# Kernel tuning notes

Measured on AMD Instinct MI355X. Metric: run time of the kernel, lower is better.

Reference implementation:

```python
import jax, jax.numpy as jnp
import numpy as np

N_AGENTS = 50000  # number of batch elements (agents); fixed num_segments
N_NEIGHBORS = 1600000  # total ragged neighbors flattened (avg degree 32)
STATE_DIM = 64
PHI_HID = 64
PHI_OUT = 64
RHO_HID = 64
ACT_DIM = 2


def setup_inputs() -> dict:
    key = jax.random.key(0)
    ks = jax.random.split(key, 6)
    s = lambda fan_in: 1.0 / np.sqrt(fan_in)
    neighbors = jax.random.normal(ks[0], (N_NEIGHBORS, STATE_DIM), dtype=jnp.float32)
    phi_w1 = jax.random.normal(ks[1], (STATE_DIM, PHI_HID), dtype=jnp.float32) * s(STATE_DIM)
    phi_b1 = jnp.zeros((PHI_HID,), dtype=jnp.float32)
    phi_w2 = jax.random.normal(ks[2], (PHI_HID, PHI_OUT), dtype=jnp.float32) * s(PHI_HID)
    phi_b2 = jnp.zeros((PHI_OUT,), dtype=jnp.float32)
    rho_w1 = jax.random.normal(ks[3], (PHI_OUT, RHO_HID), dtype=jnp.float32) * s(PHI_OUT)
    rho_b1 = jnp.zeros((RHO_HID,), dtype=jnp.float32)
    rho_w2 = jax.random.normal(ks[4], (RHO_HID, ACT_DIM), dtype=jnp.float32) * s(RHO_HID)
    rho_b2 = jnp.zeros((ACT_DIM,), dtype=jnp.float32)
    segment_ids = jnp.sort(jax.random.randint(ks[5], (N_NEIGHBORS,), 0, N_AGENTS, dtype=jnp.int32))
    return {
        "neighbors": neighbors,
        "phi_w1": phi_w1, "phi_b1": phi_b1, "phi_w2": phi_w2, "phi_b2": phi_b2,
        "rho_w1": rho_w1, "rho_b1": rho_b1, "rho_w2": rho_w2, "rho_b2": rho_b2,
        "segment_ids": segment_ids,
    }


def reference(neighbors, phi_w1, phi_b1, phi_w2, phi_b2,
              rho_w1, rho_b1, rho_w2, rho_b2, segment_ids):
    # phi MLP applied to every neighbor feature (vectorized over the flat ragged axis)
    h = jax.nn.relu(neighbors @ phi_w1 + phi_b1)          # [N_NEIGHBORS, PHI_HID]
    h = h @ phi_w2 + phi_b2                               # [N_NEIGHBORS, PHI_OUT]
    # per-agent sum over variable-length neighbor sets (the Python double loop in torch)
    summ = jax.ops.segment_sum(h, segment_ids, num_segments=N_AGENTS)  # [N_AGENTS, PHI_OUT]
    # rho MLP on pooled features
    r = jax.nn.relu(summ @ rho_w1 + rho_b1)               # [N_AGENTS, RHO_HID]
    return r @ rho_w2 + rho_b2                            # [N_AGENTS, ACT_DIM]
```

## Files before the change

### kernel.cpp

```cpp
#include <hip/hip_runtime.h>
#include <hip/hip_bf16.h>

#define N_AGENTS 50000
#define N_NEI    1600000
#define ROWS     128
#define PHI_BLOCKS (N_NEI / ROWS)

typedef __bf16 bf16_t;
typedef __attribute__((ext_vector_type(8))) __bf16 bf16x8;
typedef __attribute__((ext_vector_type(4))) __bf16 bf16x4;
typedef __attribute__((ext_vector_type(4))) float  f32x4;

#define SA 72
#define SO 66

__global__ __launch_bounds__(256) void phi_kernel(
    const float* __restrict__ nb,
    const float* __restrict__ w1g, const float* __restrict__ b1g,
    const float* __restrict__ w2g, const float* __restrict__ b2g,
    const int* __restrict__ seg, float* __restrict__ summ)
{
  __shared__ __align__(16) union {
    struct {
      bf16_t A[ROWS * SA];
      bf16_t Wt[2][64 * SA];
    } s;
    float outb[ROWS * SO];
  } u;
  __shared__ float biasf[2][64];
  __shared__ int sid[ROWS + 4];

  const int tid  = threadIdx.x;
  const int w    = tid >> 6;
  const int lane = tid & 63;
  const int m16  = lane & 15;
  const int q    = lane >> 4;
  const int base_row = blockIdx.x * ROWS;

  if (tid < ROWS) sid[tid] = seg[base_row + tid];
  if (tid < 64) biasf[0][tid] = b1g[tid];
  else if (tid < 128) biasf[1][tid - 64] = b2g[tid - 64];

  for (int i = tid; i < 4096; i += 256) {
    int k = i >> 6, n = i & 63;
    u.s.Wt[0][n * SA + k] = (bf16_t)w1g[i];
    u.s.Wt[1][n * SA + k] = (bf16_t)w2g[i];
  }

  {
    const float4* np4 = (const float4*)(nb + (size_t)base_row * 64);
    #pragma unroll
    for (int it = 0; it < 8; ++it) {
      int j = tid + it * 256;
      float4 v = np4[j];
      int row = j >> 4, col = (j & 15) * 4;
      bf16x4 p = { (bf16_t)v.x, (bf16_t)v.y, (bf16_t)v.z, (bf16_t)v.w };
      *(bf16x4*)&u.s.A[row * SA + col] = p;
    }
  }
  __syncthreads();

  const int rb = w * 32;
  bf16x8 bfr[4][2], afr[2][2];
  f32x4  acc[2][4];

  #pragma unroll
  for (int tn = 0; tn < 4; ++tn)
    #pragma unroll
    for (int kb = 0; kb < 2; ++kb)
      bfr[tn][kb] = *(const bf16x8*)&u.s.Wt[0][(tn * 16 + m16) * SA + kb * 32 + q * 8];
  #pragma unroll
  for (int tm = 0; tm < 2; ++tm)
    #pragma unroll
    for (int kb = 0; kb < 2; ++kb)
      afr[tm][kb] = *(const bf16x8*)&u.s.A[(rb + tm * 16 + m16) * SA + kb * 32 + q * 8];
  #pragma unroll
  for (int tm = 0; tm < 2; ++tm)
    #pragma unroll
    for (int tn = 0; tn < 4; ++tn) {
      f32x4 a = {0.f, 0.f, 0.f, 0.f};
      a = __builtin_amdgcn_mfma_f32_16x16x32_bf16(afr[tm][0], bfr[tn][0], a, 0, 0, 0);
      a = __builtin_amdgcn_mfma_f32_16x16x32_bf16(afr[tm][1], bfr[tn][1], a, 0, 0, 0);
      acc[tm][tn] = a;
    }
  #pragma unroll
  for (int tm = 0; tm < 2; ++tm)
    #pragma unroll
    for (int tn = 0; tn < 4; ++tn) {
      float bv = biasf[0][tn * 16 + m16];
      #pragma unroll
      for (int i = 0; i < 4; ++i) {
        float hv = fmaxf(acc[tm][tn][i] + bv, 0.f);
        u.s.A[(rb + tm * 16 + q * 4 + i) * SA + tn * 16 + m16] = (bf16_t)hv;
      }
    }

  #pragma unroll
  for (int tn = 0; tn < 4; ++tn)
    #pragma unroll
    for (int kb = 0; kb < 2; ++kb)
      bfr[tn][kb] = *(const bf16x8*)&u.s.Wt[1][(tn * 16 + m16) * SA + kb * 32 + q * 8];
  #pragma unroll
  for (int tm = 0; tm < 2; ++tm)
    #pragma unroll
    for (int kb = 0; kb < 2; ++kb)
      afr[tm][kb] = *(const bf16x8*)&u.s.A[(rb + tm * 16 + m16) * SA + kb * 32 + q * 8];
  __syncthreads();

  #pragma unroll
  for (int tm = 0; tm < 2; ++tm)
    #pragma unroll
    for (int tn = 0; tn < 4; ++tn) {
      f32x4 a = {0.f, 0.f, 0.f, 0.f};
      a = __builtin_amdgcn_mfma_f32_16x16x32_bf16(afr[tm][0], bfr[tn][0], a, 0, 0, 0);
      a = __builtin_amdgcn_mfma_f32_16x16x32_bf16(afr[tm][1], bfr[tn][1], a, 0, 0, 0);
      acc[tm][tn] = a;
    }
  #pragma unroll
  for (int tm = 0; tm < 2; ++tm)
    #pragma unroll
    for (int tn = 0; tn < 4; ++tn) {
      float bv = biasf[1][tn * 16 + m16];
      #pragma unroll
      for (int i = 0; i < 4; ++i)
        u.outb[(rb + tm * 16 + q * 4 + i) * SO + tn * 16 + m16] = acc[tm][tn][i] + bv;
    }

  float racc = 0.f;
  for (int r = rb; r < rb + 32; ++r) {
    racc += u.outb[r * SO + lane];
    int sr = sid[r];
    if (r == rb + 31 || sid[r + 1] != sr) {
      atomicAdd(summ + (size_t)sr * 64 + lane, racc);
      racc = 0.f;
    }
  }
}

__global__ __launch_bounds__(256) void rho_kernel(
    const float* __restrict__ summ,
    const float* __restrict__ w1g, const float* __restrict__ b1g,
    const float* __restrict__ w2g, const float* __restrict__ b2g,
    float* __restrict__ out)
{
  __shared__ float sw1[64 * 64];
  __shared__ float sw2[128];
  __shared__ float sb1[64];
  __shared__ float sb2[2];
  const int tid = threadIdx.x;
  for (int i = tid; i < 4096; i += 256) sw1[i] = w1g[i];
  if (tid < 128) sw2[tid] = w2g[tid];
  if (tid < 64)  sb1[tid] = b1g[tid];
  if (tid < 2)   sb2[tid] = b2g[tid];
  __syncthreads();

  int a = blockIdx.x * 256 + tid;
  if (a >= N_AGENTS) return;

  float x[64];
  const float4* xr = (const float4*)(summ + (size_t)a * 64);
  #pragma unroll
  for (int i = 0; i < 16; ++i) {
    float4 v = xr[i];
    x[4*i] = v.x; x[4*i+1] = v.y; x[4*i+2] = v.z; x[4*i+3] = v.w;
  }

  float o0 = sb2[0], o1 = sb2[1];
  for (int n = 0; n < 64; ++n) {
    float a0 = sb1[n], a1 = 0.f, a2 = 0.f, a3 = 0.f;
    #pragma unroll
    for (int k = 0; k < 64; k += 4) {
      a0 = fmaf(x[k],     sw1[(k)     * 64 + n], a0);
      a1 = fmaf(x[k + 1], sw1[(k + 1) * 64 + n], a1);
      a2 = fmaf(x[k + 2], sw1[(k + 2) * 64 + n], a2);
      a3 = fmaf(x[k + 3], sw1[(k + 3) * 64 + n], a3);
    }
    float h = fmaxf((a0 + a1) + (a2 + a3), 0.f);
    o0 = fmaf(h, sw2[2 * n],     o0);
    o1 = fmaf(h, sw2[2 * n + 1], o1);
  }
  *(float2*)(out + (size_t)a * 2) = make_float2(o0, o1);
}

extern "C" void kernel_launch(void* const* d_in, const int* in_sizes, int n_in,
                              void* d_out, int out_size, void* d_ws, size_t ws_size,
                              hipStream_t stream) {
  const float* neighbors = (const float*)d_in[0];
  const float* phi_w1    = (const float*)d_in[1];
  const float* phi_b1    = (const float*)d_in[2];
  const float* phi_w2    = (const float*)d_in[3];
  const float* phi_b2    = (const float*)d_in[4];
  const float* rho_w1    = (const float*)d_in[5];
  const float* rho_b1    = (const float*)d_in[6];
  const float* rho_w2    = (const float*)d_in[7];
  const float* rho_b2    = (const float*)d_in[8];
  const int*   seg       = (const int*)d_in[9];
  float* out  = (float*)d_out;
  float* summ = (float*)d_ws;

  hipMemsetAsync(summ, 0, (size_t)N_AGENTS * 64 * sizeof(float), stream);
  phi_kernel<<<PHI_BLOCKS, 256, 0, stream>>>(neighbors, phi_w1, phi_b1,
                                             phi_w2, phi_b2, seg, summ);
  rho_kernel<<<(N_AGENTS + 255) / 256, 256, 0, stream>>>(summ, rho_w1, rho_b1,
                                                         rho_w2, rho_b2, out);
}
```

Before: 605.1 us.

## Make phi kernel persistent with register-resident weights; transpose rho weights for vector loads

```diff
diff --git a/kernel.cpp b/kernel.cpp
--- a/kernel.cpp
+++ b/kernel.cpp
@@ -4,17 +4,17 @@
 #define N_AGENTS 50000
 #define N_NEI    1600000
 #define ROWS     128
-#define PHI_BLOCKS (N_NEI / ROWS)
+#define PHI_TILES (N_NEI / ROWS)
+#define PHI_GRID  1024
 
 typedef __bf16 bf16_t;
 typedef __attribute__((ext_vector_type(8))) __bf16 bf16x8;
-typedef __attribute__((ext_vector_type(4))) __bf16 bf16x4;
 typedef __attribute__((ext_vector_type(4))) float  f32x4;
 
 #define SA 72
 #define SO 66
 
-__global__ __launch_bounds__(256) void phi_kernel(
+__global__ __launch_bounds__(256, 3) void phi_kernel(
     const float* __restrict__ nb,
     const float* __restrict__ w1g, const float* __restrict__ b1g,
     const float* __restrict__ w2g, const float* __restrict__ b2g,
@@ -27,7 +27,6 @@
     } s;
     float outb[ROWS * SO];
   } u;
-  __shared__ float biasf[2][64];
   __shared__ int sid[ROWS + 4];
 
   const int tid  = threadIdx.x;
@@ -35,105 +34,112 @@
   const int lane = tid & 63;
   const int m16  = lane & 15;
   const int q    = lane >> 4;
-  const int base_row = blockIdx.x * ROWS;
-
-  if (tid < ROWS) sid[tid] = seg[base_row + tid];
-  if (tid < 64) biasf[0][tid] = b1g[tid];
-  else if (tid < 128) biasf[1][tid - 64] = b2g[tid - 64];
+  const int rb   = w * 32;
 
   for (int i = tid; i < 4096; i += 256) {
     int k = i >> 6, n = i & 63;
     u.s.Wt[0][n * SA + k] = (bf16_t)w1g[i];
     u.s.Wt[1][n * SA + k] = (bf16_t)w2g[i];
   }
-
-  {
-    const float4* np4 = (const float4*)(nb + (size_t)base_row * 64);
-    #pragma unroll
-    for (int it = 0; it < 8; ++it) {
-      int j = tid + it * 256;
-      float4 v = np4[j];
-      int row = j >> 4, col = (j & 15) * 4;
-      bf16x4 p = { (bf16_t)v.x, (bf16_t)v.y, (bf16_t)v.z, (bf16_t)v.w };
-      *(bf16x4*)&u.s.A[row * SA + col] = p;
-    }
+  float b1r[4], b2r[4];
+  #pragma unroll
+  for (int tn = 0; tn < 4; ++tn) {
+    b1r[tn] = b1g[tn * 16 + m16];
+    b2r[tn] = b2g[tn * 16 + m16];
   }
   __syncthreads();
 
-  const int rb = w * 32;
-  bf16x8 bfr[4][2], afr[2][2];
-  f32x4  acc[2][4];
-
+  bf16x8 bf1[4][2], bf2[4][2];
   #pragma unroll
   for (int tn = 0; tn < 4; ++tn)
     #pragma unroll
-    for (int kb = 0; kb < 2; ++kb)
-      bfr[tn][kb] = *(const bf16x8*)&u.s.Wt[0][(tn * 16 + m16) * SA + kb * 32 + q * 8];
-  #pragma unroll
-  for (int tm = 0; tm < 2; ++tm)
-    #pragma unroll
-    for (int kb = 0; kb < 2; ++kb)
-      afr[tm][kb] = *(const bf16x8*)&u.s.A[(rb + tm * 16 + m16) * SA + kb * 32 + q * 8];
-  #pragma unroll
-  for (int tm = 0; tm < 2; ++tm)
-    #pragma unroll
-    for (int tn = 0; tn < 4; ++tn) {
-      f32x4 a = {0.f, 0.f, 0.f, 0.f};
-      a = __builtin_amdgcn_mfma_f32_16x16x32_bf16(afr[tm][0], bfr[tn][0], a, 0, 0, 0);
-      a = __builtin_amdgcn_mfma_f32_16x16x32_bf16(afr[tm][1], bfr[tn][1], a, 0, 0, 0);
-      acc[tm][tn] = a;
-    }
-  #pragma unroll
-  for (int tm = 0; tm < 2; ++tm)
-    #pragma unroll
-    for (int tn = 0; tn < 4; ++tn) {
-      float bv = biasf[0][tn * 16 + m16];
-      #pragma unroll
-      for (int i = 0; i < 4; ++i) {
-        float hv = fmaxf(acc[tm][tn][i] + bv, 0.f);
-        u.s.A[(rb + tm * 16 + q * 4 + i) * SA + tn * 16 + m16] = (bf16_t)hv;
-      }
-    }
-
-  #pragma unroll
-  for (int tn = 0; tn < 4; ++tn)
-    #pragma unroll
-    for (int kb = 0; kb < 2; ++kb)
-      bfr[tn][kb] = *(const bf16x8*)&u.s.Wt[1][(tn * 16 + m16) * SA + kb * 32 + q * 8];
-  #pragma unroll
-  for (int tm = 0; tm < 2; ++tm)
-    #pragma unroll
-    for (int kb = 0; kb < 2; ++kb)
-      afr[tm][kb] = *(const bf16x8*)&u.s.A[(rb + tm * 16 + m16) * SA + kb * 32 + q * 8];
-  __syncthreads();
-
-  #pragma unroll
-  for (int tm = 0; tm < 2; ++tm)
-    #pragma unroll
-    for (int tn = 0; tn < 4; ++tn) {
-      f32x4 a = {0.f, 0.f, 0.f, 0.f};
-      a = __builtin_amdgcn_mfma_f32_16x16x32_bf16(afr[tm][0], bfr[tn][0], a, 0, 0, 0);
-      a = __builtin_amdgcn_mfma_f32_16x16x32_bf16(afr[tm][1], bfr[tn][1], a, 0, 0, 0);
-      acc[tm][tn] = a;
-    }
-  #pragma unroll
-  for (int tm = 0; tm < 2; ++tm)
-    #pragma unroll
-    for (int tn = 0; tn < 4; ++tn) {
-      float bv = biasf[1][tn * 16 + m16];
-      #pragma unroll
-      for (int i = 0; i < 4; ++i)
-        u.outb[(rb + tm * 16 + q * 4 + i) * SO + tn * 16 + m16] = acc[tm][tn][i] + bv;
-    }
-
-  float racc = 0.f;
-  for (int r = rb; r < rb + 32; ++r) {
-    racc += u.outb[r * SO + lane];
-    int sr = sid[r];
-    if (r == rb + 31 || sid[r + 1] != sr) {
-      atomicAdd(summ + (size_t)sr * 64 + lane, racc);
-      racc = 0.f;
-    }
+    for (int kb = 0; kb < 2; ++kb) {
+      bf1[tn][kb] = *(const bf16x8*)&u.s.Wt[0][(tn * 16 + m16) * SA + kb * 32 + q * 8];
+      bf2[tn][kb] = *(const bf16x8*)&u.s.Wt[1][(tn * 16 + m16) * SA + kb * 32 + q * 8];
+    }
+
+  for (int t = blockIdx.x; t < PHI_TILES; t += gridDim.x) {
+    const int base_row = t * ROWS;
+
+    if (tid < ROWS) sid[tid] = seg[base_row + tid];
+    {
+      const float4* np4 = (const float4*)(nb + (size_t)base_row * 64);
+      #pragma unroll
+      for (int it = 0; it < 4; ++it) {
+        int j = tid * 2 + it * 512;
+        float4 v0 = np4[j], v1 = np4[j + 1];
+        int row = j >> 4, col = (j & 15) * 4;
+        bf16x8 p = { (bf16_t)v0.x, (bf16_t)v0.y, (bf16_t)v0.z, (bf16_t)v0.w,
+                     (bf16_t)v1.x, (bf16_t)v1.y, (bf16_t)v1.z, (bf16_t)v1.w };
+        *(bf16x8*)&u.s.A[row * SA + col] = p;
+      }
+    }
+    __syncthreads();
+
+    bf16x8 afr[2][2];
+    f32x4  acc[2][4];
+    #pragma unroll
+    for (int tm = 0; tm < 2; ++tm)
+      #pragma unroll
+      for (int kb = 0; kb < 2; ++kb)
+        afr[tm][kb] = *(const bf16x8*)&u.s.A[(rb + tm * 16 + m16) * SA + kb * 32 + q * 8];
+    #pragma unroll
+    for (int tm = 0; tm < 2; ++tm)
+      #pragma unroll
+      for (int tn = 0; tn < 4; ++tn) {
+        f32x4 a = {0.f, 0.f, 0.f, 0.f};
+        a = __builtin_amdgcn_mfma_f32_16x16x32_bf16(afr[tm][0], bf1[tn][0], a, 0, 0, 0);
+        a = __builtin_amdgcn_mfma_f32_16x16x32_bf16(afr[tm][1], bf1[tn][1], a, 0, 0, 0);
+        acc[tm][tn] = a;
+      }
+    #pragma unroll
+    for (int tm = 0; tm < 2; ++tm)
+      #pragma unroll
+      for (int tn = 0; tn < 4; ++tn) {
+        float bv = b1r[tn];
+        #pragma unroll
+        for (int i = 0; i < 4; ++i) {
+          float hv = fmaxf(acc[tm][tn][i] + bv, 0.f);
+          u.s.A[(rb + tm * 16 + q * 4 + i) * SA + tn * 16 + m16] = (bf16_t)hv;
+        }
+      }
+
+    #pragma unroll
+    for (int tm = 0; tm < 2; ++tm)
+      #pragma unroll
+      for (int kb = 0; kb < 2; ++kb)
+        afr[tm][kb] = *(const bf16x8*)&u.s.A[(rb + tm * 16 + m16) * SA + kb * 32 + q * 8];
+    __syncthreads();
+
+    #pragma unroll
+    for (int tm = 0; tm < 2; ++tm)
+      #pragma unroll
+      for (int tn = 0; tn < 4; ++tn) {
+        f32x4 a = {0.f, 0.f, 0.f, 0.f};
+        a = __builtin_amdgcn_mfma_f32_16x16x32_bf16(afr[tm][0], bf2[tn][0], a, 0, 0, 0);
+        a = __builtin_amdgcn_mfma_f32_16x16x32_bf16(afr[tm][1], bf2[tn][1], a, 0, 0, 0);
+        acc[tm][tn] = a;
+      }
+    #pragma unroll
+    for (int tm = 0; tm < 2; ++tm)
+      #pragma unroll
+      for (int tn = 0; tn < 4; ++tn) {
+        float bv = b2r[tn];
+        #pragma unroll
+        for (int i = 0; i < 4; ++i)
+          u.outb[(rb + tm * 16 + q * 4 + i) * SO + tn * 16 + m16] = acc[tm][tn][i] + bv;
+      }
+
+    float racc = 0.f;
+    for (int r = rb; r < rb + 32; ++r) {
+      racc += u.outb[r * SO + lane];
+      int sr = sid[r];
+      if (r == rb + 31 || sid[r + 1] != sr) {
+        atomicAdd(summ + (size_t)sr * 64 + lane, racc);
+        racc = 0.f;
+      }
+    }
+    __syncthreads();
   }
 }
 
@@ -143,12 +149,15 @@
     const float* __restrict__ w2g, const float* __restrict__ b2g,
     float* __restrict__ out)
 {
-  __shared__ float sw1[64 * 64];
+  __shared__ float sw1t[64 * 68];
   __shared__ float sw2[128];
   __shared__ float sb1[64];
   __shared__ float sb2[2];
   const int tid = threadIdx.x;
-  for (int i = tid; i < 4096; i += 256) sw1[i] = w1g[i];
+  for (int i = tid; i < 4096; i += 256) {
+    int n = i >> 6, k = i & 63;
+    sw1t[n * 68 + k] = w1g[k * 64 + n];
+  }
   if (tid < 128) sw2[tid] = w2g[tid];
   if (tid < 64)  sb1[tid] = b1g[tid];
   if (tid < 2)   sb2[tid] = b2g[tid];
@@ -167,13 +176,15 @@
 
   float o0 = sb2[0], o1 = sb2[1];
   for (int n = 0; n < 64; ++n) {
+    const float4* wr = (const float4*)&sw1t[n * 68];
     float a0 = sb1[n], a1 = 0.f, a2 = 0.f, a3 = 0.f;
     #pragma unroll
-    for (int k = 0; k < 64; k += 4) {
-      a0 = fmaf(x[k],     sw1[(k)     * 64 + n], a0);
-      a1 = fmaf(x[k + 1], sw1[(k + 1) * 64 + n], a1);
-      a2 = fmaf(x[k + 2], sw1[(k + 2) * 64 + n], a2);
-      a3 = fmaf(x[k + 3], sw1[(k + 3) * 64 + n], a3);
+    for (int kq = 0; kq < 16; ++kq) {
+      float4 wv = wr[kq];
+      a0 = fmaf(x[4*kq],     wv.x, a0);
+      a1 = fmaf(x[4*kq + 1], wv.y, a1);
+      a2 = fmaf(x[4*kq + 2], wv.z, a2);
+      a3 = fmaf(x[4*kq + 3], wv.w, a3);
     }
     float h = fmaxf((a0 + a1) + (a2 + a3), 0.f);
     o0 = fmaf(h, sw2[2 * n],     o0);
@@ -199,8 +210,8 @@
   float* summ = (float*)d_ws;
 
   hipMemsetAsync(summ, 0, (size_t)N_AGENTS * 64 * sizeof(float), stream);
-  phi_kernel<<<PHI_BLOCKS, 256, 0, stream>>>(neighbors, phi_w1, phi_b1,
-                                             phi_w2, phi_b2, seg, summ);
+  phi_kernel<<<PHI_GRID, 256, 0, stream>>>(neighbors, phi_w1, phi_b1,
+                                           phi_w2, phi_b2, seg, summ);
   rho_kernel<<<(N_AGENTS + 255) / 256, 256, 0, stream>>>(summ, rho_w1, rho_b1,
                                                          rho_w2, rho_b2, out);
 }
```

Measured after the change: 628.1 us. +3.8%, slower.
